# Kernel optimization log

Measured on AMD Instinct MI355X. Metric: run time of the kernel, lower is better.

## Reference

```python
import jax, jax.numpy as jnp
import numpy as np


def _dct_matrix():
    # 8-point DCT-II basis, H[i,j] = c_i * cos(i*(2j+1)*pi/16), c_0=sqrt(1/8), else sqrt(2/8)
    i = np.arange(8, dtype=np.float64)[:, None]
    j = np.arange(8, dtype=np.float64)[None, :]
    H = np.sqrt(2.0 / 8.0) * np.cos(i * (2.0 * j + 1.0) * np.pi / 16.0)
    H[0, :] = np.sqrt(1.0 / 8.0)  # cos(0)=1 for i==0 row
    return jnp.asarray(H, dtype=jnp.float32)


def setup_inputs() -> dict:
    key = jax.random.key(0)
    x = jax.random.normal(key, (16, 192, 128, 128), dtype=jnp.float32)
    return {"x": x, "H": _dct_matrix(), "opt": 0}


def reference(x, H, opt):
    if opt:
        # DCT path: [B, C, Hh, Ww] -> [B, C*64, Hh//8, Ww//8]
        B, C, Hh, Ww = x.shape
        Hb, Wb = Hh // 8, Ww // 8
        blocks = x.reshape(B, C, Hb, 8, Wb, 8)  # (b,c,hb,i,wb,j)
        # per-block H @ block @ H^T
        y = jnp.einsum('pi,bchiwj,qj->bcpqhw', H, blocks, H)
        return y.reshape(B, C * 64, Hb, Wb)
    else:
        # IDCT path: [B, C*64, Hb, Wb] -> [B, C, Hb*8, Wb*8]
        B, C64, Hb, Wb = x.shape
        C = C64 // 64
        blocks = x.reshape(B, C, 8, 8, Hb, Wb)  # (b,c,i,j,hb,wb)
        # per-block H^T @ block @ H
        y = jnp.einsum('ip,bcijhw,jq->bchpwq', H, blocks, H)
        return y.reshape(B, C, Hb * 8, Wb * 8)
```

## Files before the change

kernel.cpp:

```cpp
#include <hip/hip_runtime.h>


#define PLANE 16384

__global__ __launch_bounds__(256) void idct_kernel(const float* __restrict__ x,
                                                   const float* __restrict__ Hm,
                                                   float* __restrict__ out) {
    __shared__ float Hs[64];
    __shared__ __align__(16) float T[8 * 8 * 128];

    const int t = threadIdx.x;
    if (t < 64) Hs[t] = Hm[t];

    const int bc = blockIdx.x >> 7;
    const int hb = blockIdx.x & 127;

    __syncthreads();

    {
        const int j = t >> 5;
        const int g = t & 31;
        const float* src = x + (size_t)(bc * 64 + j) * PLANE + hb * 128 + g * 4;
        float4 v[8];
#pragma unroll
        for (int i = 0; i < 8; ++i)
            v[i] = *(const float4*)(src + (size_t)i * (8 * PLANE));
#pragma unroll
        for (int p = 0; p < 8; ++p) {
            float4 acc = make_float4(0.f, 0.f, 0.f, 0.f);
#pragma unroll
            for (int i = 0; i < 8; ++i) {
                float h = Hs[i * 8 + p];
                acc.x = fmaf(h, v[i].x, acc.x);
                acc.y = fmaf(h, v[i].y, acc.y);
                acc.z = fmaf(h, v[i].z, acc.z);
                acc.w = fmaf(h, v[i].w, acc.w);
            }
            *(float4*)&T[p * 1024 + j * 128 + g * 4] = acc;
        }
    }

    __syncthreads();

    {
        const int p = t >> 5;
        const int g = t & 31;
        const int q0 = (g & 1) * 4;
        const int wb0 = g >> 1;

        float hq[8][4];
#pragma unroll
        for (int j = 0; j < 8; ++j)
#pragma unroll
            for (int c = 0; c < 4; ++c) hq[j][c] = Hs[j * 8 + q0 + c];

        float* dst = out + (size_t)bc * (1024u * 1024u) + (size_t)(hb * 8 + p) * 1024;
#pragma unroll
        for (int k = 0; k < 8; ++k) {
            const int wb = wb0 + 16 * k;
            float tj[8];
#pragma unroll
            for (int j = 0; j < 8; ++j) tj[j] = T[p * 1024 + j * 128 + wb];
            float4 o = make_float4(0.f, 0.f, 0.f, 0.f);
#pragma unroll
            for (int j = 0; j < 8; ++j) {
                o.x = fmaf(tj[j], hq[j][0], o.x);
                o.y = fmaf(tj[j], hq[j][1], o.y);
                o.z = fmaf(tj[j], hq[j][2], o.z);
                o.w = fmaf(tj[j], hq[j][3], o.w);
            }
            *(float4*)(dst + (size_t)(g + 32 * k) * 4) = o;
        }
    }
}

extern "C" void kernel_launch(void* const* d_in, const int* in_sizes, int n_in,
                              void* d_out, int out_size, void* d_ws, size_t ws_size,
                              hipStream_t stream) {
    const float* x = (const float*)d_in[0];
    const float* H = (const float*)d_in[1];
    float* out = (float*)d_out;

    idct_kernel<<<48 * 128, 256, 0, stream>>>(x, H, out);
}
```

Measured before the change: 77.73 us.

## Process multiple block-rows per workgroup with register prefetch and nontemporal stores

Each workgroup now handles four consecutive block-rows, prefetching the next row's input into registers while computing and storing the current row's output. Output stores use nontemporal hints to avoid polluting cache, and phase-one DCT coefficients are read directly from global memory as uniform values. This aims to overlap load latency with compute and amortize setup, at the cost of four times fewer workgroups and extra barriers per row.

Result: faster. 65.75 us (-15.4%).

```diff
diff --git a/kernel.cpp b/kernel.cpp
--- a/kernel.cpp
+++ b/kernel.cpp
@@ -2,6 +2,9 @@
 
 
 #define PLANE 16384
+#define ROWS 4
+
+typedef float vf4 __attribute__((ext_vector_type(4)));
 
 __global__ __launch_bounds__(256) void idct_kernel(const float* __restrict__ x,
                                                    const float* __restrict__ Hm,
@@ -10,66 +13,75 @@
     __shared__ __align__(16) float T[8 * 8 * 128];
 
     const int t = threadIdx.x;
+    const int bc = blockIdx.x >> 5;
+    const int hb0 = (blockIdx.x & 31) * ROWS;
+
+    const int j1 = t >> 5, g1 = t & 31;
+    const int p2 = j1, g2 = g1;
+    const int q0 = (g2 & 1) * 4;
+    const int wb0 = g2 >> 1;
+
     if (t < 64) Hs[t] = Hm[t];
 
-    const int bc = blockIdx.x >> 7;
-    const int hb = blockIdx.x & 127;
+    const float* src = x + (size_t)(bc * 64 + j1) * PLANE + hb0 * 128 + g1 * 4;
 
-    __syncthreads();
-
-    {
-        const int j = t >> 5;
-        const int g = t & 31;
-        const float* src = x + (size_t)(bc * 64 + j) * PLANE + hb * 128 + g * 4;
-        float4 v[8];
+    float4 v[8];
+    auto loadrow = [&](int r) {
 #pragma unroll
         for (int i = 0; i < 8; ++i)
-            v[i] = *(const float4*)(src + (size_t)i * (8 * PLANE));
+            v[i] = *(const float4*)(src + (size_t)r * 128 + (size_t)i * (8 * PLANE));
+    };
+    auto phase1 = [&]() {
 #pragma unroll
         for (int p = 0; p < 8; ++p) {
             float4 acc = make_float4(0.f, 0.f, 0.f, 0.f);
 #pragma unroll
             for (int i = 0; i < 8; ++i) {
-                float h = Hs[i * 8 + p];
+                float h = Hm[i * 8 + p];
                 acc.x = fmaf(h, v[i].x, acc.x);
                 acc.y = fmaf(h, v[i].y, acc.y);
                 acc.z = fmaf(h, v[i].z, acc.z);
                 acc.w = fmaf(h, v[i].w, acc.w);
             }
-            *(float4*)&T[p * 1024 + j * 128 + g * 4] = acc;
+            *(float4*)&T[p * 1024 + j1 * 128 + g1 * 4] = acc;
         }
-    }
+    };
 
+    loadrow(0);
+    phase1();
     __syncthreads();
 
-    {
-        const int p = t >> 5;
-        const int g = t & 31;
-        const int q0 = (g & 1) * 4;
-        const int wb0 = g >> 1;
+    float4 hq[8];
+#pragma unroll
+    for (int j = 0; j < 8; ++j) hq[j] = *(const float4*)&Hs[j * 8 + q0];
 
-        float hq[8][4];
 #pragma unroll
-        for (int j = 0; j < 8; ++j)
-#pragma unroll
-            for (int c = 0; c < 4; ++c) hq[j][c] = Hs[j * 8 + q0 + c];
+    for (int r = 0; r < ROWS; ++r) {
+        if (r + 1 < ROWS) loadrow(r + 1);
 
-        float* dst = out + (size_t)bc * (1024u * 1024u) + (size_t)(hb * 8 + p) * 1024;
+        float* dst = out + (size_t)bc * (1024u * 1024u) + (size_t)((hb0 + r) * 8 + p2) * 1024;
 #pragma unroll
         for (int k = 0; k < 8; ++k) {
             const int wb = wb0 + 16 * k;
             float tj[8];
 #pragma unroll
-            for (int j = 0; j < 8; ++j) tj[j] = T[p * 1024 + j * 128 + wb];
-            float4 o = make_float4(0.f, 0.f, 0.f, 0.f);
+            for (int j = 0; j < 8; ++j) tj[j] = T[p2 * 1024 + j * 128 + wb];
+            float o0 = 0.f, o1 = 0.f, o2 = 0.f, o3 = 0.f;
 #pragma unroll
             for (int j = 0; j < 8; ++j) {
-                o.x = fmaf(tj[j], hq[j][0], o.x);
-                o.y = fmaf(tj[j], hq[j][1], o.y);
-                o.z = fmaf(tj[j], hq[j][2], o.z);
-                o.w = fmaf(tj[j], hq[j][3], o.w);
+                o0 = fmaf(tj[j], hq[j].x, o0);
+                o1 = fmaf(tj[j], hq[j].y, o1);
+                o2 = fmaf(tj[j], hq[j].z, o2);
+                o3 = fmaf(tj[j], hq[j].w, o3);
             }
-            *(float4*)(dst + (size_t)(g + 32 * k) * 4) = o;
+            vf4 o = {o0, o1, o2, o3};
+            __builtin_nontemporal_store(o, (vf4*)(dst + (size_t)(g2 + 32 * k) * 4));
+        }
+
+        if (r + 1 < ROWS) {
+            __syncthreads();
+            phase1();
+            __syncthreads();
         }
     }
 }
@@ -81,5 +93,5 @@
     const float* H = (const float*)d_in[1];
     float* out = (float*)d_out;
 
-    idct_kernel<<<48 * 128, 256, 0, stream>>>(x, H, out);
+    idct_kernel<<<48 * (128 / ROWS), 256, 0, stream>>>(x, H, out);
 }
```
